# Optimization experiments

Measured on AMD Instinct MI355X. Metric: run time of the kernel, lower is better.

Reference implementation:

```python
import jax, jax.numpy as jnp
import numpy as np

N = 100000   # nodes
E = 1600000  # edges
IN, H, OUT = 128, 128, 64
EPS = 1e-5   # BatchNorm1d eps


def setup_inputs() -> dict:
    key = jax.random.key(0)
    ks = jax.random.split(key, 6)
    glorot = lambda k, i, o: jax.random.normal(k, (i, o), jnp.float32) / np.float32(np.sqrt(i))
    return {
        "x": jax.random.normal(ks[0], (N, IN), jnp.float32),
        "edge_index": jax.random.randint(ks[1], (2, E), 0, N, dtype=jnp.int32),
        "W1": glorot(ks[2], IN, H),
        "b1": jnp.zeros((H,), jnp.float32),
        "g1": jnp.ones((H,), jnp.float32),
        "be1": jnp.zeros((H,), jnp.float32),
        "W2": glorot(ks[3], H, H),
        "b2": jnp.zeros((H,), jnp.float32),
        "g2": jnp.ones((H,), jnp.float32),
        "be2": jnp.zeros((H,), jnp.float32),
        "W3": glorot(ks[4], H, OUT),
        "b3": jnp.zeros((OUT,), jnp.float32),
    }


def _gcn_conv(x, W, b, src, dst, dinv):
    # PyG GCNConv: h = x @ W (no linear bias); symmetric-normalized scatter-add
    # over edges with implicit self-loops; then additive bias.
    h = x @ W                                           # [N, F]
    coef = (dinv[src] * dinv[dst])[:, None]             # [E, 1]
    agg = jax.ops.segment_sum(h[src] * coef, dst, num_segments=N)
    agg = agg + h * (dinv * dinv)[:, None]              # self-loop term
    return agg + b


def _bn(x, g, b):
    # BatchNorm1d, training-mode batch statistics (biased variance).
    m = jnp.mean(x, axis=0)
    v = jnp.mean(jnp.square(x - m), axis=0)
    return (x - m) * jax.lax.rsqrt(v + EPS) * g + b


def reference(x, edge_index, W1, b1, g1, be1, W2, b2, g2, be2, W3, b3):
    src, dst = edge_index[0], edge_index[1]
    # degree with self-loops (edge weights = 1)
    deg = jax.ops.segment_sum(jnp.ones((E,), jnp.float32), dst, num_segments=N) + 1.0
    dinv = jax.lax.rsqrt(deg)

    x1 = jax.nn.relu(_bn(_gcn_conv(x, W1, b1, src, dst, dinv), g1, be1))
    x2 = jax.nn.relu(_bn(_gcn_conv(x1, W2, b2, src, dst, dinv), g2, be2))
    x2 = x2 + x1                                        # skip connection
    return _gcn_conv(x2, W3, b3, src, dst, dinv)
```

## Files before the change

kernel.cpp:

```cpp
#include <hip/hip_runtime.h>

#define BN_EPS 1e-5f

typedef unsigned short ushort_t;
typedef __attribute__((ext_vector_type(8))) short bf16x8;
typedef __attribute__((ext_vector_type(16))) float f32x16;

__device__ __forceinline__ ushort_t bf16rne(float f) {
    unsigned int u = __float_as_uint(f);
    unsigned int r = (u + 0x7FFFu + ((u >> 16) & 1u)) >> 16;
    return (ushort_t)r;
}
__device__ __forceinline__ unsigned int pack2(float a, float b) {
    return (unsigned int)bf16rne(a) | ((unsigned int)bf16rne(b) << 16);
}
__device__ __forceinline__ void cvt2(unsigned int u, float& lo, float& hi) {
    lo = __uint_as_float(u << 16);
    hi = __uint_as_float(u & 0xFFFF0000u);
}
__device__ __forceinline__ bf16x8 as_bf16x8(uint4 u) {
    union { uint4 u; bf16x8 v; } c; c.u = u; return c.v;
}


#define BIN_CHUNK 4096

__global__ __launch_bounds__(256) void k_binhist(const int* __restrict__ dst, int E, int NB,
                                                 int* __restrict__ bucket_counts) {
    __shared__ int hist[512];
    for (int i = threadIdx.x; i < NB; i += 256) hist[i] = 0;
    __syncthreads();
    int base = blockIdx.x * BIN_CHUNK;
    int end = min(E, base + BIN_CHUNK);
    for (int e = base + threadIdx.x; e < end; e += 256)
        atomicAdd(&hist[dst[e] >> 8], 1);
    __syncthreads();
    for (int i = threadIdx.x; i < NB; i += 256)
        if (hist[i]) atomicAdd(&bucket_counts[i], hist[i]);
}

__global__ void k_bucketscan(const int* __restrict__ bucket_counts, int NB, int N, int E,
                             int* __restrict__ bucket_base, int* __restrict__ bucket_cursor,
                             int* __restrict__ rowptr) {
    __shared__ int sh[512];
    int t = threadIdx.x;
    int v = (t < NB) ? bucket_counts[t] : 0;
    sh[t] = v;
    __syncthreads();
    for (int off = 1; off < 512; off <<= 1) {
        int x = (t >= off) ? sh[t - off] : 0;
        __syncthreads();
        sh[t] += x;
        __syncthreads();
    }
    if (t < NB) {
        int b = sh[t] - v;
        bucket_base[t] = b;
        bucket_cursor[t] = b;
    }
    if (t == 0) { bucket_base[NB] = E; rowptr[N] = E; }
}

__global__ __launch_bounds__(256) void k_bin(const int* __restrict__ src,
                                             const int* __restrict__ dst, int E, int NB,
                                             int* __restrict__ bucket_cursor,
                                             int2* __restrict__ binned) {
    __shared__ int hist[512];
    __shared__ int cur[512];
    for (int i = threadIdx.x; i < NB; i += 256) hist[i] = 0;
    __syncthreads();
    int base = blockIdx.x * BIN_CHUNK;
    int end = min(E, base + BIN_CHUNK);
    for (int e = base + threadIdx.x; e < end; e += 256)
        atomicAdd(&hist[dst[e] >> 8], 1);
    __syncthreads();
    for (int i = threadIdx.x; i < NB; i += 256)
        cur[i] = hist[i] ? atomicAdd(&bucket_cursor[i], hist[i]) : 0;
    __syncthreads();
    for (int e = base + threadIdx.x; e < end; e += 256) {
        int d = dst[e];
        int pos = atomicAdd(&cur[d >> 8], 1);
        binned[pos] = make_int2(src[e], d);
    }
}

__global__ __launch_bounds__(256) void k_bucket(const int2* __restrict__ binned,
                                                const int* __restrict__ bucket_base, int N,
                                                int* __restrict__ rowptr,
                                                float* __restrict__ dinv,
                                                int* __restrict__ csr_src) {
    __shared__ int cnt[256];
    __shared__ int sh[256];
    __shared__ int cur[256];
    int b = blockIdx.x;
    int t = threadIdx.x;
    int node0 = b << 8;
    int lo = bucket_base[b], hi = bucket_base[b + 1];
    cnt[t] = 0;
    __syncthreads();
    for (int p = lo + t; p < hi; p += 256) {
        int2 pr = binned[p];
        atomicAdd(&cnt[pr.y & 255], 1);
    }
    __syncthreads();
    int v = cnt[t];
    sh[t] = v;
    __syncthreads();
    for (int off = 1; off < 256; off <<= 1) {
        int y = (t >= off) ? sh[t - off] : 0;
        __syncthreads();
        sh[t] += y;
        __syncthreads();
    }
    int gbase = lo + (sh[t] - v);
    int node = node0 + t;
    if (node < N) {
        rowptr[node] = gbase;
        dinv[node] = rsqrtf((float)v + 1.0f);
    }
    cur[t] = gbase;
    __syncthreads();
    for (int p = lo + t; p < hi; p += 256) {
        int2 pr = binned[p];
        int pos = atomicAdd(&cur[pr.y & 255], 1);
        csr_src[pos] = pr.x;
    }
}


__global__ void k_bnparam(const float* __restrict__ sp, const float* __restrict__ g,
                          const float* __restrict__ be, float* __restrict__ scale,
                          float* __restrict__ shift, float invN) {
    int j = threadIdx.x;
    float s = 0.f, q = 0.f;
#pragma unroll
    for (int w = 0; w < 32; ++w) {
        s += sp[w * 128 + j];
        q += sp[32 * 128 + w * 128 + j];
    }
    float m = s * invN;
    float var = q * invN - m * m;
    float r = rsqrtf(var + BN_EPS);
    float sc = g[j] * r;
    scale[j] = sc;
    shift[j] = be[j] - m * sc;
}


__global__ void k_wprep(const float* __restrict__ W, ushort_t* __restrict__ BT, int M) {
    int col = blockIdx.x;
    int k = threadIdx.x;
    BT[col * 128 + k] = bf16rne(W[k * M + col]);
}

__global__ __launch_bounds__(256) void k_xcvt(const float* __restrict__ X,
                                              ushort_t* __restrict__ Xb, int total8) {
    int i = blockIdx.x * 256 + threadIdx.x;
    if (i >= total8) return;
    float4 a = ((const float4*)X)[2 * i];
    float4 b = ((const float4*)X)[2 * i + 1];
    uint4 po;
    po.x = pack2(a.x, a.y); po.y = pack2(a.z, a.w);
    po.z = pack2(b.x, b.y); po.w = pack2(b.z, b.w);
    ((uint4*)Xb)[i] = po;
}

template<bool ADDSKIP>
__global__ __launch_bounds__(256) void k_bntrans(const ushort_t* __restrict__ Ain,
                                                 const float* __restrict__ scale,
                                                 const float* __restrict__ shift,
                                                 const ushort_t* __restrict__ skip,
                                                 ushort_t* __restrict__ Outb, int N) {
    int i = blockIdx.x * 256 + threadIdx.x;
    if (i >= N * 16) return;
    int j0 = (i & 15) * 8;
    uint4 raw = ((const uint4*)Ain)[i];
    float v[8];
    cvt2(raw.x, v[0], v[1]); cvt2(raw.y, v[2], v[3]);
    cvt2(raw.z, v[4], v[5]); cvt2(raw.w, v[6], v[7]);
    float4 sc0 = *(const float4*)&scale[j0];
    float4 sc1 = *(const float4*)&scale[j0 + 4];
    float4 sh0 = *(const float4*)&shift[j0];
    float4 sh1 = *(const float4*)&shift[j0 + 4];
    v[0] = fmaxf(v[0] * sc0.x + sh0.x, 0.f);
    v[1] = fmaxf(v[1] * sc0.y + sh0.y, 0.f);
    v[2] = fmaxf(v[2] * sc0.z + sh0.z, 0.f);
    v[3] = fmaxf(v[3] * sc0.w + sh0.w, 0.f);
    v[4] = fmaxf(v[4] * sc1.x + sh1.x, 0.f);
    v[5] = fmaxf(v[5] * sc1.y + sh1.y, 0.f);
    v[6] = fmaxf(v[6] * sc1.z + sh1.z, 0.f);
    v[7] = fmaxf(v[7] * sc1.w + sh1.w, 0.f);
    if constexpr (ADDSKIP) {
        uint4 s4 = ((const uint4*)skip)[i];
        float lo, hi;
        cvt2(s4.x, lo, hi); v[0] += lo; v[1] += hi;
        cvt2(s4.y, lo, hi); v[2] += lo; v[3] += hi;
        cvt2(s4.z, lo, hi); v[4] += lo; v[5] += hi;
        cvt2(s4.w, lo, hi); v[6] += lo; v[7] += hi;
    }
    uint4 po;
    po.x = pack2(v[0], v[1]); po.y = pack2(v[2], v[3]);
    po.z = pack2(v[4], v[5]); po.w = pack2(v[6], v[7]);
    ((uint4*)Outb)[i] = po;
}


template<int M>
__global__ __launch_bounds__(256) void k_mgemm(const ushort_t* __restrict__ A,
                                               const ushort_t* __restrict__ BT,
                                               ushort_t* __restrict__ Out, int N) {
    constexpr int CT = M / 32;
    int wid = threadIdx.x >> 6;
    int lane = threadIdx.x & 63;
    int l31 = lane & 31;
    int khalf = (lane >> 5) * 8;
    int rowbase = blockIdx.x * 128 + wid * 32;
    int arow = rowbase + l31;

    f32x16 acc[CT] = {};

#pragma unroll
    for (int ks = 0; ks < 8; ++ks) {
        bf16x8 af = {};
        if (arow < N)
            af = as_bf16x8(*(const uint4*)&A[(size_t)arow * 128 + ks * 16 + khalf]);
#pragma unroll
        for (int ct = 0; ct < CT; ++ct) {
            int bcol = ct * 32 + l31;
            bf16x8 bfr = as_bf16x8(*(const uint4*)&BT[(size_t)bcol * 128 + ks * 16 + khalf]);
            acc[ct] = __builtin_amdgcn_mfma_f32_32x32x16_bf16(af, bfr, acc[ct], 0, 0, 0);
        }
    }

#pragma unroll
    for (int ct = 0; ct < CT; ++ct) {
        int col = ct * 32 + l31;
#pragma unroll
        for (int q = 0; q < 16; ++q) {
            int row = rowbase + (q & 3) + 8 * (q >> 2) + 4 * (lane >> 5);
            if (row < N)
                Out[(size_t)row * M + col] = bf16rne(acc[ct][q]);
        }
    }
}


template<int M, bool STATS, bool BF16OUT>
__global__ __launch_bounds__(256) void k_agg(const ushort_t* __restrict__ Hm,
                      const int* __restrict__ rowptr,
                      const int* __restrict__ csr_src, const float* __restrict__ dinv,
                      const float* __restrict__ bias, void* __restrict__ Out, int N,
                      float* __restrict__ spread) {
    constexpr int TPN = M / 8;
    constexpr int NPB = 256 / TPN;
    int li = threadIdx.x / TPN;
    int lane = threadIdx.x % TPN;
    int i = blockIdx.x * NPB + li;
    bool valid = (i < N);
    int j0 = lane * 8;

    float o[8] = {0.f, 0.f, 0.f, 0.f, 0.f, 0.f, 0.f, 0.f};

    if (valid) {
        int p = rowptr[i], p1 = rowptr[i + 1];
        for (; p + 3 < p1; p += 4) {
            int s0 = csr_src[p + 0];
            int s1 = csr_src[p + 1];
            int s2 = csr_src[p + 2];
            int s3 = csr_src[p + 3];
            float c0 = dinv[s0], c1 = dinv[s1], c2 = dinv[s2], c3 = dinv[s3];
            uint4 g0 = *(const uint4*)&Hm[(size_t)s0 * M + j0];
            uint4 g1 = *(const uint4*)&Hm[(size_t)s1 * M + j0];
            uint4 g2 = *(const uint4*)&Hm[(size_t)s2 * M + j0];
            uint4 g3 = *(const uint4*)&Hm[(size_t)s3 * M + j0];
            float lo, hi;
            cvt2(g0.x, lo, hi); o[0] += lo * c0; o[1] += hi * c0;
            cvt2(g0.y, lo, hi); o[2] += lo * c0; o[3] += hi * c0;
            cvt2(g0.z, lo, hi); o[4] += lo * c0; o[5] += hi * c0;
            cvt2(g0.w, lo, hi); o[6] += lo * c0; o[7] += hi * c0;
            cvt2(g1.x, lo, hi); o[0] += lo * c1; o[1] += hi * c1;
            cvt2(g1.y, lo, hi); o[2] += lo * c1; o[3] += hi * c1;
            cvt2(g1.z, lo, hi); o[4] += lo * c1; o[5] += hi * c1;
            cvt2(g1.w, lo, hi); o[6] += lo * c1; o[7] += hi * c1;
            cvt2(g2.x, lo, hi); o[0] += lo * c2; o[1] += hi * c2;
            cvt2(g2.y, lo, hi); o[2] += lo * c2; o[3] += hi * c2;
            cvt2(g2.z, lo, hi); o[4] += lo * c2; o[5] += hi * c2;
            cvt2(g2.w, lo, hi); o[6] += lo * c2; o[7] += hi * c2;
            cvt2(g3.x, lo, hi); o[0] += lo * c3; o[1] += hi * c3;
            cvt2(g3.y, lo, hi); o[2] += lo * c3; o[3] += hi * c3;
            cvt2(g3.z, lo, hi); o[4] += lo * c3; o[5] += hi * c3;
            cvt2(g3.w, lo, hi); o[6] += lo * c3; o[7] += hi * c3;
        }
        for (; p < p1; ++p) {
            int s = csr_src[p];
            float cf = dinv[s];
            uint4 g = *(const uint4*)&Hm[(size_t)s * M + j0];
            float lo, hi;
            cvt2(g.x, lo, hi); o[0] += lo * cf; o[1] += hi * cf;
            cvt2(g.y, lo, hi); o[2] += lo * cf; o[3] += hi * cf;
            cvt2(g.z, lo, hi); o[4] += lo * cf; o[5] += hi * cf;
            cvt2(g.w, lo, hi); o[6] += lo * cf; o[7] += hi * cf;
        }

        float di = dinv[i];
        uint4 hs = *(const uint4*)&Hm[(size_t)i * M + j0];
        float lo, hi;
        cvt2(hs.x, lo, hi); o[0] += lo * di; o[1] += hi * di;
        cvt2(hs.y, lo, hi); o[2] += lo * di; o[3] += hi * di;
        cvt2(hs.z, lo, hi); o[4] += lo * di; o[5] += hi * di;
        cvt2(hs.w, lo, hi); o[6] += lo * di; o[7] += hi * di;

        float4 bv0 = *(const float4*)&bias[j0];
        float4 bv1 = *(const float4*)&bias[j0 + 4];
        o[0] = o[0] * di + bv0.x; o[1] = o[1] * di + bv0.y;
        o[2] = o[2] * di + bv0.z; o[3] = o[3] * di + bv0.w;
        o[4] = o[4] * di + bv1.x; o[5] = o[5] * di + bv1.y;
        o[6] = o[6] * di + bv1.z; o[7] = o[7] * di + bv1.w;
    }

    if constexpr (STATS) {
        float st[16];
#pragma unroll
        for (int k = 0; k < 8; ++k) { st[k] = o[k]; st[8 + k] = o[k] * o[k]; }
#pragma unroll
        for (int k = 0; k < 16; ++k) {
            st[k] += __shfl_xor(st[k], 16);
            st[k] += __shfl_xor(st[k], 32);
        }
        __shared__ float red[4][16][16];
        int wv = threadIdx.x >> 6;
        int ln = threadIdx.x & 63;
        if (ln < 16) {
#pragma unroll
            for (int k = 0; k < 16; ++k) red[wv][ln][k] = st[k];
        }
        __syncthreads();
        if (threadIdx.x < 16) {
            int cg = threadIdx.x;
            int w = (blockIdx.x & 31);
#pragma unroll
            for (int k = 0; k < 16; ++k) {
                float s = red[0][cg][k] + red[1][cg][k] + red[2][cg][k] + red[3][cg][k];
                int j = cg * 8 + (k & 7);
                float* dst = (k < 8) ? &spread[w * 128 + j]
                                     : &spread[32 * 128 + w * 128 + j];
                atomicAdd(dst, s);
            }
        }
    }

    if constexpr (BF16OUT) {
        if (valid) {
            uint4 po;
            po.x = pack2(o[0], o[1]); po.y = pack2(o[2], o[3]);
            po.z = pack2(o[4], o[5]); po.w = pack2(o[6], o[7]);
            *(uint4*)&((ushort_t*)Out)[(size_t)i * M + j0] = po;
        }
    } else {
        __shared__ float outs[NPB][M + 4];
#pragma unroll
        for (int cc = 0; cc < 8; ++cc) outs[li][lane * 8 + cc] = o[cc];
        __syncthreads();
        float* Of = (float*)Out;
        int i0 = blockIdx.x * NPB;
        constexpr int Q = M / 4;
        for (int f = threadIdx.x; f < NPB * Q; f += 256) {
            int node = f / Q;
            int q = f % Q;
            if (i0 + node < N)
                *(float4*)&Of[(size_t)(i0 + node) * M + q * 4] = *(float4*)&outs[node][q * 4];
        }
    }
}


extern "C" void kernel_launch(void* const* d_in, const int* in_sizes, int n_in,
                              void* d_out, int out_size, void* d_ws, size_t ws_size,
                              hipStream_t stream) {
    const float* x   = (const float*)d_in[0];
    const int*   ei  = (const int*)d_in[1];
    const float* W1  = (const float*)d_in[2];
    const float* b1  = (const float*)d_in[3];
    const float* g1  = (const float*)d_in[4];
    const float* be1 = (const float*)d_in[5];
    const float* W2  = (const float*)d_in[6];
    const float* b2  = (const float*)d_in[7];
    const float* g2  = (const float*)d_in[8];
    const float* be2 = (const float*)d_in[9];
    const float* W3  = (const float*)d_in[10];
    const float* b3  = (const float*)d_in[11];

    int N = in_sizes[0] / 128;
    int E = in_sizes[1] / 2;
    const int* srcp = ei;
    const int* dstp = ei + E;
    int NB = (N + 255) >> 8;

    char* ws = (char*)d_ws;
    size_t off = 0;
    auto alloc = [&](size_t bytes) {
        void* p = ws + off;
        off += (bytes + 255) & ~(size_t)255;
        return p;
    };

    int*   rowptr   = (int*)alloc(((size_t)N + 1) * 4);
    int*   csr_src  = (int*)alloc((size_t)E * 4);
    float* dinv     = (float*)alloc((size_t)N * 4);
    int*   bucket_counts = (int*)alloc(512 * 4);
    int*   bucket_base   = (int*)alloc(513 * 4);
    int*   bucket_cursor = (int*)alloc(512 * 4);
    float* spreadA  = (float*)alloc(2 * 32 * 128 * 4);
    float* spreadB  = (float*)alloc(2 * 32 * 128 * 4);
    float* scale1   = (float*)alloc(128 * 4);
    float* shift1   = (float*)alloc(128 * 4);
    float* scale2   = (float*)alloc(128 * 4);
    float* shift2   = (float*)alloc(128 * 4);
    ushort_t* BT1   = (ushort_t*)alloc(128 * 128 * 2);
    ushort_t* BT2   = (ushort_t*)alloc(128 * 128 * 2);
    ushort_t* BT3   = (ushort_t*)alloc(64 * 128 * 2);
    ushort_t* xbf   = (ushort_t*)alloc((size_t)N * 128 * 2);
    ushort_t* hbuf  = (ushort_t*)alloc((size_t)N * 128 * 2);
    ushort_t* x1bf  = (ushort_t*)alloc((size_t)N * 128 * 2);
    ushort_t* x2bf  = (ushort_t*)alloc((size_t)N * 128 * 2);
    ushort_t* abuf1 = (ushort_t*)alloc((size_t)N * 128 * 2);
    ushort_t* abuf2 = (ushort_t*)alloc((size_t)N * 128 * 2);
    int2*  binned = (int2*)abuf1;

    float invN = 1.0f / (float)N;
    int nbE = (E + BIN_CHUNK - 1) / BIN_CHUNK;
    int gemmBlocks = (N + 127) / 128;
    int ncvt8 = N * 16;

    hipMemsetAsync(bucket_counts, 0, 512 * 4, stream);
    k_binhist<<<nbE, 256, 0, stream>>>(dstp, E, NB, bucket_counts);
    k_bucketscan<<<1, 512, 0, stream>>>(bucket_counts, NB, N, E,
                                        bucket_base, bucket_cursor, rowptr);
    k_bin<<<nbE, 256, 0, stream>>>(srcp, dstp, E, NB, bucket_cursor, binned);
    k_bucket<<<NB, 256, 0, stream>>>(binned, bucket_base, N, rowptr, dinv, csr_src);
    hipMemsetAsync(spreadA, 0, 2 * 32 * 128 * 4, stream);
    hipMemsetAsync(spreadB, 0, 2 * 32 * 128 * 4, stream);

    k_wprep<<<128, 128, 0, stream>>>(W1, BT1, 128);
    k_wprep<<<128, 128, 0, stream>>>(W2, BT2, 128);
    k_wprep<<<64, 128, 0, stream>>>(W3, BT3, 64);
    k_xcvt<<<(ncvt8 + 255) / 256, 256, 0, stream>>>(x, xbf, ncvt8);

    k_mgemm<128><<<gemmBlocks, 256, 0, stream>>>(xbf, BT1, hbuf, N);
    k_agg<128, true, true><<<(N + 15) / 16, 256, 0, stream>>>(hbuf, rowptr, csr_src, dinv,
                                                              b1, abuf1, N, spreadA);
    k_bnparam<<<1, 128, 0, stream>>>(spreadA, g1, be1, scale1, shift1, invN);

    k_bntrans<false><<<(ncvt8 + 255) / 256, 256, 0, stream>>>(abuf1, scale1, shift1,
                                                              nullptr, x1bf, N);
    k_mgemm<128><<<gemmBlocks, 256, 0, stream>>>(x1bf, BT2, hbuf, N);
    k_agg<128, true, true><<<(N + 15) / 16, 256, 0, stream>>>(hbuf, rowptr, csr_src, dinv,
                                                              b2, abuf2, N, spreadB);
    k_bnparam<<<1, 128, 0, stream>>>(spreadB, g2, be2, scale2, shift2, invN);

    k_bntrans<true><<<(ncvt8 + 255) / 256, 256, 0, stream>>>(abuf2, scale2, shift2,
                                                             x1bf, x2bf, N);
    k_mgemm<64><<<gemmBlocks, 256, 0, stream>>>(x2bf, BT3, hbuf, N);
    k_agg<64, false, false><<<(N + 31) / 32, 256, 0, stream>>>(hbuf, rowptr, csr_src, dinv,
                                                               b3, d_out, N, nullptr);
}
```

Measured before the change: 436.2 us.

## Fuse BN/ReLU/skip and fp32 conversion into GEMM prologue; pack binned edges

Removes the standalone x-to-bf16 conversion and the two BN-transform kernels by applying the conversion, BN scale/shift, ReLU and skip-add inside the GEMM's A-operand load. The x1/x2 intermediate buffers are no longer written and re-read. BN statistics now go as per-block partial sums into a buffer, reduced by a new small kernel, replacing contended global atomics. Edge binning packs the source index and the low 8 bits of dst into one 32-bit word, halving that traffic. The risks are that the GEMM re-derives x1 from abuf1 with extra ALU work in MODE 2, and the packing assumes node indices fit in 24 bits.

```diff
diff --git a/kernel.cpp b/kernel.cpp
--- a/kernel.cpp
+++ b/kernel.cpp
@@ -20,6 +20,12 @@
 }
 __device__ __forceinline__ bf16x8 as_bf16x8(uint4 u) {
     union { uint4 u; bf16x8 v; } c; c.u = u; return c.v;
+}
+__device__ __forceinline__ bf16x8 pack8(const float v[8]) {
+    union { uint4 u; bf16x8 b; } c;
+    c.u.x = pack2(v[0], v[1]); c.u.y = pack2(v[2], v[3]);
+    c.u.z = pack2(v[4], v[5]); c.u.w = pack2(v[6], v[7]);
+    return c.b;
 }
 
 
@@ -64,7 +70,7 @@
 __global__ __launch_bounds__(256) void k_bin(const int* __restrict__ src,
                                              const int* __restrict__ dst, int E, int NB,
                                              int* __restrict__ bucket_cursor,
-                                             int2* __restrict__ binned) {
+                                             unsigned int* __restrict__ binned) {
     __shared__ int hist[512];
     __shared__ int cur[512];
     for (int i = threadIdx.x; i < NB; i += 256) hist[i] = 0;
@@ -80,11 +86,11 @@
     for (int e = base + threadIdx.x; e < end; e += 256) {
         int d = dst[e];
         int pos = atomicAdd(&cur[d >> 8], 1);
-        binned[pos] = make_int2(src[e], d);
-    }
-}
-
-__global__ __launch_bounds__(256) void k_bucket(const int2* __restrict__ binned,
+        binned[pos] = (unsigned int)src[e] | ((unsigned int)(d & 255) << 24);
+    }
+}
+
+__global__ __launch_bounds__(256) void k_bucket(const unsigned int* __restrict__ binned,
                                                 const int* __restrict__ bucket_base, int N,
                                                 int* __restrict__ rowptr,
                                                 float* __restrict__ dinv,
@@ -98,10 +104,8 @@
     int lo = bucket_base[b], hi = bucket_base[b + 1];
     cnt[t] = 0;
     __syncthreads();
-    for (int p = lo + t; p < hi; p += 256) {
-        int2 pr = binned[p];
-        atomicAdd(&cnt[pr.y & 255], 1);
-    }
+    for (int p = lo + t; p < hi; p += 256)
+        atomicAdd(&cnt[binned[p] >> 24], 1);
     __syncthreads();
     int v = cnt[t];
     sh[t] = v;
@@ -121,23 +125,29 @@
     cur[t] = gbase;
     __syncthreads();
     for (int p = lo + t; p < hi; p += 256) {
-        int2 pr = binned[p];
-        int pos = atomicAdd(&cur[pr.y & 255], 1);
-        csr_src[pos] = pr.x;
-    }
-}
-
-
-__global__ void k_bnparam(const float* __restrict__ sp, const float* __restrict__ g,
+        unsigned int pr = binned[p];
+        int pos = atomicAdd(&cur[pr >> 24], 1);
+        csr_src[pos] = (int)(pr & 0xFFFFFFu);
+    }
+}
+
+
+__global__ __launch_bounds__(256) void k_statreduce(const float* __restrict__ partial,
+                                                    int nblk, float* __restrict__ sp256) {
+    int t = threadIdx.x;
+    float acc = 0.f;
+    for (int r = blockIdx.x; r < nblk; r += 32)
+        acc += partial[(size_t)r * 256 + t];
+    atomicAdd(&sp256[t], acc);
+}
+
+__global__ void k_bnparam(const float* __restrict__ sp256, const float* __restrict__ g,
                           const float* __restrict__ be, float* __restrict__ scale,
                           float* __restrict__ shift, float invN) {
     int j = threadIdx.x;
-    float s = 0.f, q = 0.f;
-#pragma unroll
-    for (int w = 0; w < 32; ++w) {
-        s += sp[w * 128 + j];
-        q += sp[32 * 128 + w * 128 + j];
-    }
+    int cg = j >> 3, klo = j & 7;
+    float s = sp256[(klo << 4) | cg];
+    float q = sp256[((klo + 8) << 4) | cg];
     float m = s * invN;
     float var = q * invN - m * m;
     float r = rsqrtf(var + BN_EPS);
@@ -153,62 +163,16 @@
     BT[col * 128 + k] = bf16rne(W[k * M + col]);
 }
 
-__global__ __launch_bounds__(256) void k_xcvt(const float* __restrict__ X,
-                                              ushort_t* __restrict__ Xb, int total8) {
-    int i = blockIdx.x * 256 + threadIdx.x;
-    if (i >= total8) return;
-    float4 a = ((const float4*)X)[2 * i];
-    float4 b = ((const float4*)X)[2 * i + 1];
-    uint4 po;
-    po.x = pack2(a.x, a.y); po.y = pack2(a.z, a.w);
-    po.z = pack2(b.x, b.y); po.w = pack2(b.z, b.w);
-    ((uint4*)Xb)[i] = po;
-}
-
-template<bool ADDSKIP>
-__global__ __launch_bounds__(256) void k_bntrans(const ushort_t* __restrict__ Ain,
-                                                 const float* __restrict__ scale,
-                                                 const float* __restrict__ shift,
-                                                 const ushort_t* __restrict__ skip,
-                                                 ushort_t* __restrict__ Outb, int N) {
-    int i = blockIdx.x * 256 + threadIdx.x;
-    if (i >= N * 16) return;
-    int j0 = (i & 15) * 8;
-    uint4 raw = ((const uint4*)Ain)[i];
-    float v[8];
-    cvt2(raw.x, v[0], v[1]); cvt2(raw.y, v[2], v[3]);
-    cvt2(raw.z, v[4], v[5]); cvt2(raw.w, v[6], v[7]);
-    float4 sc0 = *(const float4*)&scale[j0];
-    float4 sc1 = *(const float4*)&scale[j0 + 4];
-    float4 sh0 = *(const float4*)&shift[j0];
-    float4 sh1 = *(const float4*)&shift[j0 + 4];
-    v[0] = fmaxf(v[0] * sc0.x + sh0.x, 0.f);
-    v[1] = fmaxf(v[1] * sc0.y + sh0.y, 0.f);
-    v[2] = fmaxf(v[2] * sc0.z + sh0.z, 0.f);
-    v[3] = fmaxf(v[3] * sc0.w + sh0.w, 0.f);
-    v[4] = fmaxf(v[4] * sc1.x + sh1.x, 0.f);
-    v[5] = fmaxf(v[5] * sc1.y + sh1.y, 0.f);
-    v[6] = fmaxf(v[6] * sc1.z + sh1.z, 0.f);
-    v[7] = fmaxf(v[7] * sc1.w + sh1.w, 0.f);
-    if constexpr (ADDSKIP) {
-        uint4 s4 = ((const uint4*)skip)[i];
-        float lo, hi;
-        cvt2(s4.x, lo, hi); v[0] += lo; v[1] += hi;
-        cvt2(s4.y, lo, hi); v[2] += lo; v[3] += hi;
-        cvt2(s4.z, lo, hi); v[4] += lo; v[5] += hi;
-        cvt2(s4.w, lo, hi); v[6] += lo; v[7] += hi;
-    }
-    uint4 po;
-    po.x = pack2(v[0], v[1]); po.y = pack2(v[2], v[3]);
-    po.z = pack2(v[4], v[5]); po.w = pack2(v[6], v[7]);
-    ((uint4*)Outb)[i] = po;
-}
-
-
-template<int M>
-__global__ __launch_bounds__(256) void k_mgemm(const ushort_t* __restrict__ A,
+
+template<int M, int MODE>
+__global__ __launch_bounds__(256) void k_mgemm(const void* __restrict__ Av,
+                                               const ushort_t* __restrict__ A1b,
                                                const ushort_t* __restrict__ BT,
-                                               ushort_t* __restrict__ Out, int N) {
+                                               ushort_t* __restrict__ Out, int N,
+                                               const float* __restrict__ scale2,
+                                               const float* __restrict__ shift2,
+                                               const float* __restrict__ scale1,
+                                               const float* __restrict__ shift1) {
     constexpr int CT = M / 32;
     int wid = threadIdx.x >> 6;
     int lane = threadIdx.x & 63;
@@ -221,9 +185,54 @@
 
 #pragma unroll
     for (int ks = 0; ks < 8; ++ks) {
+        int j0 = ks * 16 + khalf;
         bf16x8 af = {};
-        if (arow < N)
-            af = as_bf16x8(*(const uint4*)&A[(size_t)arow * 128 + ks * 16 + khalf]);
+        if (arow < N) {
+            if constexpr (MODE == 0) {
+                const float* X = (const float*)Av;
+                float4 a = *(const float4*)&X[(size_t)arow * 128 + j0];
+                float4 b = *(const float4*)&X[(size_t)arow * 128 + j0 + 4];
+                float v[8] = {a.x, a.y, a.z, a.w, b.x, b.y, b.z, b.w};
+                af = pack8(v);
+            } else {
+                const ushort_t* X = (const ushort_t*)Av;
+                uint4 raw = *(const uint4*)&X[(size_t)arow * 128 + j0];
+                float v[8];
+                cvt2(raw.x, v[0], v[1]); cvt2(raw.y, v[2], v[3]);
+                cvt2(raw.z, v[4], v[5]); cvt2(raw.w, v[6], v[7]);
+                float4 sc0 = *(const float4*)&scale2[j0];
+                float4 sc1 = *(const float4*)&scale2[j0 + 4];
+                float4 sh0 = *(const float4*)&shift2[j0];
+                float4 sh1 = *(const float4*)&shift2[j0 + 4];
+                v[0] = fmaxf(v[0] * sc0.x + sh0.x, 0.f);
+                v[1] = fmaxf(v[1] * sc0.y + sh0.y, 0.f);
+                v[2] = fmaxf(v[2] * sc0.z + sh0.z, 0.f);
+                v[3] = fmaxf(v[3] * sc0.w + sh0.w, 0.f);
+                v[4] = fmaxf(v[4] * sc1.x + sh1.x, 0.f);
+                v[5] = fmaxf(v[5] * sc1.y + sh1.y, 0.f);
+                v[6] = fmaxf(v[6] * sc1.z + sh1.z, 0.f);
+                v[7] = fmaxf(v[7] * sc1.w + sh1.w, 0.f);
+                if constexpr (MODE == 2) {
+                    uint4 r1 = *(const uint4*)&A1b[(size_t)arow * 128 + j0];
+                    float w[8];
+                    cvt2(r1.x, w[0], w[1]); cvt2(r1.y, w[2], w[3]);
+                    cvt2(r1.z, w[4], w[5]); cvt2(r1.w, w[6], w[7]);
+                    float4 tc0 = *(const float4*)&scale1[j0];
+                    float4 tc1 = *(const float4*)&scale1[j0 + 4];
+                    float4 th0 = *(const float4*)&shift1[j0];
+                    float4 th1 = *(const float4*)&shift1[j0 + 4];
+                    v[0] += fmaxf(w[0] * tc0.x + th0.x, 0.f);
+                    v[1] += fmaxf(w[1] * tc0.y + th0.y, 0.f);
+                    v[2] += fmaxf(w[2] * tc0.z + th0.z, 0.f);
+                    v[3] += fmaxf(w[3] * tc0.w + th0.w, 0.f);
+                    v[4] += fmaxf(w[4] * tc1.x + th1.x, 0.f);
+                    v[5] += fmaxf(w[5] * tc1.y + th1.y, 0.f);
+                    v[6] += fmaxf(w[6] * tc1.z + th1.z, 0.f);
+                    v[7] += fmaxf(w[7] * tc1.w + th1.w, 0.f);
+                }
+                af = pack8(v);
+            }
+        }
 #pragma unroll
         for (int ct = 0; ct < CT; ++ct) {
             int bcol = ct * 32 + l31;
@@ -250,7 +259,7 @@
                       const int* __restrict__ rowptr,
                       const int* __restrict__ csr_src, const float* __restrict__ dinv,
                       const float* __restrict__ bias, void* __restrict__ Out, int N,
-                      float* __restrict__ spread) {
+                      float* __restrict__ partial) {
     constexpr int TPN = M / 8;
     constexpr int NPB = 256 / TPN;
     int li = threadIdx.x / TPN;
@@ -335,17 +344,11 @@
             for (int k = 0; k < 16; ++k) red[wv][ln][k] = st[k];
         }
         __syncthreads();
-        if (threadIdx.x < 16) {
-            int cg = threadIdx.x;
-            int w = (blockIdx.x & 31);
-#pragma unroll
-            for (int k = 0; k < 16; ++k) {
-                float s = red[0][cg][k] + red[1][cg][k] + red[2][cg][k] + red[3][cg][k];
-                int j = cg * 8 + (k & 7);
-                float* dst = (k < 8) ? &spread[w * 128 + j]
-                                     : &spread[32 * 128 + w * 128 + j];
-                atomicAdd(dst, s);
-            }
+        {
+            int t = threadIdx.x;
+            int cg = t & 15, k = t >> 4;
+            float s = red[0][cg][k] + red[1][cg][k] + red[2][cg][k] + red[3][cg][k];
+            partial[(size_t)blockIdx.x * 256 + t] = s;
         }
     }
 
@@ -404,14 +407,18 @@
         return p;
     };
 
+    int nblk128 = (N + 15) / 16;
+
     int*   rowptr   = (int*)alloc(((size_t)N + 1) * 4);
     int*   csr_src  = (int*)alloc((size_t)E * 4);
     float* dinv     = (float*)alloc((size_t)N * 4);
     int*   bucket_counts = (int*)alloc(512 * 4);
     int*   bucket_base   = (int*)alloc(513 * 4);
     int*   bucket_cursor = (int*)alloc(512 * 4);
-    float* spreadA  = (float*)alloc(2 * 32 * 128 * 4);
-    float* spreadB  = (float*)alloc(2 * 32 * 128 * 4);
+    float* partialA = (float*)alloc((size_t)nblk128 * 256 * 4);
+    float* partialB = (float*)alloc((size_t)nblk128 * 256 * 4);
+    float* sp256A   = (float*)alloc(256 * 4);
+    float* sp256B   = (float*)alloc(256 * 4);
     float* scale1   = (float*)alloc(128 * 4);
     float* shift1   = (float*)alloc(128 * 4);
     float* scale2   = (float*)alloc(128 * 4);
@@ -419,18 +426,14 @@
     ushort_t* BT1   = (ushort_t*)alloc(128 * 128 * 2);
     ushort_t* BT2   = (ushort_t*)alloc(128 * 128 * 2);
     ushort_t* BT3   = (ushort_t*)alloc(64 * 128 * 2);
-    ushort_t* xbf   = (ushort_t*)alloc((size_t)N * 128 * 2);
     ushort_t* hbuf  = (ushort_t*)alloc((size_t)N * 128 * 2);
-    ushort_t* x1bf  = (ushort_t*)alloc((size_t)N * 128 * 2);
-    ushort_t* x2bf  = (ushort_t*)alloc((size_t)N * 128 * 2);
     ushort_t* abuf1 = (ushort_t*)alloc((size_t)N * 128 * 2);
     ushort_t* abuf2 = (ushort_t*)alloc((size_t)N * 128 * 2);
-    int2*  binned = (int2*)abuf1;
+    unsigned int* binned = (unsigned int*)abuf1;
 
     float invN = 1.0f / (float)N;
     int nbE = (E + BIN_CHUNK - 1) / BIN_CHUNK;
     int gemmBlocks = (N + 127) / 128;
-    int ncvt8 = N * 16;
 
     hipMemsetAsync(bucket_counts, 0, 512 * 4, stream);
     k_binhist<<<nbE, 256, 0, stream>>>(dstp, E, NB, bucket_counts);
@@ -438,29 +441,29 @@
                                         bucket_base, bucket_cursor, rowptr);
     k_bin<<<nbE, 256, 0, stream>>>(srcp, dstp, E, NB, bucket_cursor, binned);
     k_bucket<<<NB, 256, 0, stream>>>(binned, bucket_base, N, rowptr, dinv, csr_src);
-    hipMemsetAsync(spreadA, 0, 2 * 32 * 128 * 4, stream);
-    hipMemsetAsync(spreadB, 0, 2 * 32 * 128 * 4, stream);
+    hipMemsetAsync(sp256A, 0, 256 * 4, stream);
+    hipMemsetAsync(sp256B, 0, 256 * 4, stream);
 
     k_wprep<<<128, 128, 0, stream>>>(W1, BT1, 128);
     k_wprep<<<128, 128, 0, stream>>>(W2, BT2, 128);
     k_wprep<<<64, 128, 0, stream>>>(W3, BT3, 64);
-    k_xcvt<<<(ncvt8 + 255) / 256, 256, 0, stream>>>(x, xbf, ncvt8);
-
-    k_mgemm<128><<<gemmBlocks, 256, 0, stream>>>(xbf, BT1, hbuf, N);
-    k_agg<128, true, true><<<(N + 15) / 16, 256, 0, stream>>>(hbuf, rowptr, csr_src, dinv,
-                                                              b1, abuf1, N, spreadA);
-    k_bnparam<<<1, 128, 0, stream>>>(spreadA, g1, be1, scale1, shift1, invN);
-
-    k_bntrans<false><<<(ncvt8 + 255) / 256, 256, 0, stream>>>(abuf1, scale1, shift1,
-                                                              nullptr, x1bf, N);
-    k_mgemm<128><<<gemmBlocks, 256, 0, stream>>>(x1bf, BT2, hbuf, N);
-    k_agg<128, true, true><<<(N + 15) / 16, 256, 0, stream>>>(hbuf, rowptr, csr_src, dinv,
-                                                              b2, abuf2, N, spreadB);
-    k_bnparam<<<1, 128, 0, stream>>>(spreadB, g2, be2, scale2, shift2, invN);
-
-    k_bntrans<true><<<(ncvt8 + 255) / 256, 256, 0, stream>>>(abuf2, scale2, shift2,
-                                                             x1bf, x2bf, N);
-    k_mgemm<64><<<gemmBlocks, 256, 0, stream>>>(x2bf, BT3, hbuf, N);
+
+    k_mgemm<128, 0><<<gemmBlocks, 256, 0, stream>>>(x, nullptr, BT1, hbuf, N,
+                                                    nullptr, nullptr, nullptr, nullptr);
+    k_agg<128, true, true><<<nblk128, 256, 0, stream>>>(hbuf, rowptr, csr_src, dinv,
+                                                        b1, abuf1, N, partialA);
+    k_statreduce<<<32, 256, 0, stream>>>(partialA, nblk128, sp256A);
+    k_bnparam<<<1, 128, 0, stream>>>(sp256A, g1, be1, scale1, shift1, invN);
+
+    k_mgemm<128, 1><<<gemmBlocks, 256, 0, stream>>>(abuf1, nullptr, BT2, hbuf, N,
+                                                    scale1, shift1, nullptr, nullptr);
+    k_agg<128, true, true><<<nblk128, 256, 0, stream>>>(hbuf, rowptr, csr_src, dinv,
+                                                        b2, abuf2, N, partialB);
+    k_statreduce<<<32, 256, 0, stream>>>(partialB, nblk128, sp256B);
+    k_bnparam<<<1, 128, 0, stream>>>(sp256B, g2, be2, scale2, shift2, invN);
+
+    k_mgemm<64, 2><<<gemmBlocks, 256, 0, stream>>>(abuf2, abuf1, BT3, hbuf, N,
+                                                   scale2, shift2, scale1, shift1);
     k_agg<64, false, false><<<(N + 31) / 32, 256, 0, stream>>>(hbuf, rowptr, csr_src, dinv,
                                                                b3, d_out, N, nullptr);
 }
```

Result: slower. 445.3 us (+2.1%).
